# Kernel optimization log

Hardware: AMD Instinct MI355X
Metric: run time of the kernel (lower is better)

## Reference

```python
import jax, jax.numpy as jnp
from jax import lax
import numpy as np

ALPHA = 0.82
MAXITER = 10
N1_NODES = 2048
N2_NODES = 2048
K_ATTR = 64
EDGE_P = 0.004  # sparse-ish adjacency density


def setup_inputs() -> dict:
    key = jax.random.key(0)
    k1, k2, k3, k4 = jax.random.split(key, 4)
    A1 = (jax.random.uniform(k1, (N1_NODES, N1_NODES)) < EDGE_P).astype(jnp.float32)
    A1 = jnp.maximum(A1, A1.T)  # undirected 0/1 adjacency
    A2 = (jax.random.uniform(k2, (N2_NODES, N2_NODES)) < EDGE_P).astype(jnp.float32)
    A2 = jnp.maximum(A2, A2.T)
    N1 = jax.random.uniform(k3, (N1_NODES, K_ATTR), dtype=jnp.float32)
    N2 = jax.random.uniform(k4, (N2_NODES, K_ATTR), dtype=jnp.float32)
    # default prior (_get_H with path=None), normalized so sum ~= 1
    H = jnp.full((N2_NODES, N1_NODES), 1.0 / (N1_NODES * N2_NODES), dtype=jnp.float32)
    return {"A1": A1, "A2": A2, "N1": N1, "N2": N2, "H": H}


def _row_l2_normalize(N):
    nrm = jnp.sqrt(jnp.sum(N * N, axis=1, keepdims=True))
    return jnp.where(nrm > 0, N / jnp.where(nrm > 0, nrm, 1.0), 0.0)


def _final_forward(A1, A2, N1, N2, H, alpha=ALPHA, maxiter=MAXITER):
    # No edge attrs: L=1, E1=A1, E2=A2. T = 1/A^2 where A^2>0 (elementwise),
    # E <- E*T, so B = (E*A) = A*T*A.
    def masked_recip_sq(A):
        A2e = A * A
        return jnp.where(A2e > 0, 1.0 / jnp.where(A2e > 0, A2e, 1.0), 0.0)

    B1 = (A1 * masked_recip_sq(A1)) * A1  # (n1, n1)
    B2 = (A2 * masked_recip_sq(A2)) * A2  # (n2, n2)

    N1n = _row_l2_normalize(N1)  # (n1, K)
    N2n = _row_l2_normalize(N2)  # (n2, K)

    # Kronecker vectors laid out as (n1, n2) matrices (C-order == kron order):
    # N[i*n2+j] = sum_k N1[i,k]*N2[j,k]  -> N1n @ N2n.T
    Nm = N1n @ N2n.T  # (n1, n2)
    dm = (B1 @ N1n) @ (B2 @ N2n).T  # (n1, n2)
    D = Nm * dm
    DD = jnp.where(D > 0, lax.rsqrt(jnp.where(D > 0, D, 1.0)), 0.0)  # inf -> 0
    q = DD * Nm  # (n1, n2)

    # h = H.flatten('F') with H (n2,n1): as an (n1,n2) matrix this is H.T
    h = H.T  # (n1, n2)

    def step(s, _):
        # M = (q*s) reshaped (n2,n1) F-order == (q*s).T in our layout.
        # S = B2 @ M @ B1 (n2,n1); S.flatten('F') as (n1,n2) == B1.T @ (q*s) @ B2.T
        S_t = B1.T @ (q * s) @ B2.T  # (n1, n2)
        s_new = (1.0 - alpha) * h + alpha * q * S_t
        return s_new, None

    s, _ = lax.scan(step, h, None, length=maxiter)
    # original: s.reshape((n1, n2)) C-order -> exactly our layout
    return s  # (n1, n2) alignment matrix


def reference(A1, A2, N1, N2, H):
    return _final_forward(A1, A2, N1, N2, H)
```

## Files before the change

kernel.cpp:

```cpp
#include <hip/hip_runtime.h>

#define NMAT 2048
#define KATTR 64
#define CAP 128
#define NITER 10
#define NSTRIPE 128
#define LSTRIDE 9

typedef unsigned short ushort4v __attribute__((ext_vector_type(4)));

__device__ __forceinline__ unsigned short f2bf(float f) {
  unsigned u = __float_as_uint(f);
  return (unsigned short)((u + 0x7fff + ((u >> 16) & 1)) >> 16);
}
__device__ __forceinline__ float bf2f(unsigned short b) {
  return __uint_as_float((unsigned)b << 16);
}
__device__ __forceinline__ float bflo(unsigned v) {
  return __uint_as_float(v << 16);
}
__device__ __forceinline__ float bfhi(unsigned v) {
  return __uint_as_float(v & 0xffff0000u);
}
__device__ __forceinline__ int swz(int c) { return 4 * c + (((c >> 3) & 7) << 2); }
__device__ __forceinline__ size_t bidx(int i, int j) {
  return ((size_t)(j >> 4) * NMAT + i) * 16 + (j & 15);
}

__global__ __launch_bounds__(256) void k_build(
    const float* __restrict__ A, unsigned short* __restrict__ idx,
    unsigned short* __restrict__ idxT, int* __restrict__ cnt) {
  __shared__ int lcnt;
  int r = blockIdx.x;
  if (threadIdx.x == 0) lcnt = 0;
  __syncthreads();
  const float* row = A + (size_t)r * NMAT;
  for (int c = threadIdx.x; c < NMAT; c += 256) {
    if (row[c] != 0.0f) {
      int p = atomicAdd(&lcnt, 1);
      if (p < CAP) {
        idx[r * CAP + p] = (unsigned short)c;
        if (idxT) idxT[(size_t)p * NMAT + r] = (unsigned short)c;
      }
    }
  }
  __syncthreads();
  if (threadIdx.x == 0) cnt[r] = lcnt < CAP ? lcnt : CAP;
}

__global__ __launch_bounds__(256) void k_norm(const float* __restrict__ Nin,
                                              float* __restrict__ Nout) {
  int row = blockIdx.x * 4 + (threadIdx.x >> 6);
  int lane = threadIdx.x & 63;
  float v = Nin[(size_t)row * KATTR + lane];
  float ss = v * v;
#pragma unroll
  for (int o = 32; o > 0; o >>= 1) ss += __shfl_xor(ss, o);
  float nrm = sqrtf(ss);
  Nout[(size_t)row * KATTR + lane] = (nrm > 0.f) ? v / nrm : 0.f;
}

__global__ void k_gatherN(const unsigned short* __restrict__ idx,
                          const int* __restrict__ cnt,
                          const float* __restrict__ Nn,
                          float* __restrict__ C) {
  int i = blockIdx.x;
  int lane = threadIdx.x;
  int nn = cnt[i];
  const unsigned short* ip = idx + i * CAP;
  float acc = 0.f;
  for (int t = 0; t < nn; ++t) {
    int k = ip[t];
    acc += Nn[(size_t)k * KATTR + lane];
  }
  C[(size_t)i * KATTR + lane] = acc;
}

__global__ __launch_bounds__(256) void k_transpose(const float* __restrict__ H,
                                                   float* __restrict__ Ht) {
  __shared__ float tile[64][65];
  int j0 = blockIdx.x * 64;
  int i0 = blockIdx.y * 64;
  int c = threadIdx.x & 63;
  int r0 = threadIdx.x >> 6;
  for (int r = r0; r < 64; r += 4)
    tile[r][c] = H[(size_t)(j0 + r) * NMAT + i0 + c];
  __syncthreads();
  for (int r = r0; r < 64; r += 4)
    Ht[(size_t)(i0 + r) * NMAT + j0 + c] = tile[c][r];
}

__global__ __launch_bounds__(256) void k_q(
    const float* __restrict__ N1n, const float* __restrict__ C1,
    const float* __restrict__ N2n, const float* __restrict__ C2,
    const float* __restrict__ Ht, float* __restrict__ q,
    float* __restrict__ Q2, unsigned short* __restrict__ Mblk,
    unsigned short* __restrict__ M0base) {
  __shared__ float sA[64][68];
  __shared__ float sB[64][68];
  int i0 = blockIdx.y * 64, j0 = blockIdx.x * 64;
  int c = threadIdx.x & 63, r0 = threadIdx.x >> 6;
  int tx = threadIdx.x & 15, ty = threadIdx.x >> 4;
  const float alpha = 0.82f;

  float nmv[4][4] = {};
  float dmv[4][4] = {};

  for (int r = r0; r < 64; r += 4) {
    sA[c][r] = N1n[(size_t)(i0 + r) * KATTR + c];
    sB[c][r] = N2n[(size_t)(j0 + r) * KATTR + c];
  }
  __syncthreads();
#pragma unroll 4
  for (int k = 0; k < 64; ++k) {
    float4 a = *(const float4*)&sA[k][ty * 4];
    float4 b = *(const float4*)&sB[k][tx * 4];
    float av[4] = {a.x, a.y, a.z, a.w};
    float bv[4] = {b.x, b.y, b.z, b.w};
#pragma unroll
    for (int ii = 0; ii < 4; ++ii)
#pragma unroll
      for (int jj = 0; jj < 4; ++jj)
        nmv[ii][jj] = fmaf(av[ii], bv[jj], nmv[ii][jj]);
  }
  __syncthreads();
  for (int r = r0; r < 64; r += 4) {
    sA[c][r] = C1[(size_t)(i0 + r) * KATTR + c];
    sB[c][r] = C2[(size_t)(j0 + r) * KATTR + c];
  }
  __syncthreads();
#pragma unroll 4
  for (int k = 0; k < 64; ++k) {
    float4 a = *(const float4*)&sA[k][ty * 4];
    float4 b = *(const float4*)&sB[k][tx * 4];
    float av[4] = {a.x, a.y, a.z, a.w};
    float bv[4] = {b.x, b.y, b.z, b.w};
#pragma unroll
    for (int ii = 0; ii < 4; ++ii)
#pragma unroll
      for (int jj = 0; jj < 4; ++jj)
        dmv[ii][jj] = fmaf(av[ii], bv[jj], dmv[ii][jj]);
  }

#pragma unroll
  for (int ii = 0; ii < 4; ++ii) {
    int i = i0 + ty * 4 + ii;
    int jb = j0 + tx * 4;
    size_t base = (size_t)i * NMAT + jb;
    float4 hv = *(const float4*)&Ht[base];
    float hvv[4] = {hv.x, hv.y, hv.z, hv.w};
    float qv[4], q2v[4];
    ushort4v mv, m0v;
#pragma unroll
    for (int jj = 0; jj < 4; ++jj) {
      float nmx = nmv[ii][jj];
      float D = nmx * dmv[ii][jj];
      float qq = (D > 0.f) ? nmx * rsqrtf(D) : 0.f;
      qv[jj] = qq;
      q2v[jj] = alpha * qq * qq;
      float m0 = qq * hvv[jj];
      mv[jj] = f2bf(m0);
      m0v[jj] = f2bf((1.0f - alpha) * m0);
    }
    *(float4*)&q[base] = make_float4(qv[0], qv[1], qv[2], qv[3]);
    *(float4*)&Q2[base] = make_float4(q2v[0], q2v[1], q2v[2], q2v[3]);
    *(ushort4v*)&Mblk[bidx(i, jb)] = mv;
    *(ushort4v*)&M0base[base] = m0v;
  }
}

__global__ __launch_bounds__(1024, 8) void k1s(
    const unsigned short* __restrict__ idx1, const int* __restrict__ cnt1,
    const unsigned short* __restrict__ Mblk, float* __restrict__ T1) {
  __shared__ unsigned lds[NMAT * LSTRIDE];
  int stripe = blockIdx.x & (NSTRIPE - 1);
  int chunk = blockIdx.x >> 7;
  int tid = threadIdx.x;
  const unsigned* src = (const unsigned*)(Mblk + (size_t)stripe * NMAT * 16);
#pragma unroll
  for (int p = 0; p < 4; ++p) {
    int e = p * 4096 + tid * 4;
    uint4 v = *(const uint4*)(src + e);
    int row = e >> 3;
    int cc = e & 7;
    lds[row * LSTRIDE + cc] = v.x;
    lds[row * LSTRIDE + cc + 1] = v.y;
    lds[row * LSTRIDE + cc + 2] = v.z;
    lds[row * LSTRIDE + cc + 3] = v.w;
  }
  __syncthreads();

  int i = chunk * 512 + (tid >> 1);
  int h = tid & 1;
  int nn = cnt1[i];
  const unsigned short* ip = idx1 + i * CAP;
  float a0 = 0, a1 = 0, a2 = 0, a3 = 0, a4 = 0, a5 = 0, a6 = 0, a7 = 0;
  int t = 0;
  for (; t + 2 <= nn; t += 2) {
    unsigned pr = *(const unsigned*)(ip + t);
    int ka = (int)(pr & 0xffff) * LSTRIDE + h * 4;
    int kb = (int)(pr >> 16) * LSTRIDE + h * 4;
    unsigned w0 = lds[ka], w1 = lds[ka + 1], w2 = lds[ka + 2], w3 = lds[ka + 3];
    unsigned x0 = lds[kb], x1 = lds[kb + 1], x2 = lds[kb + 2], x3 = lds[kb + 3];
    a0 += bflo(w0) + bflo(x0); a1 += bfhi(w0) + bfhi(x0);
    a2 += bflo(w1) + bflo(x1); a3 += bfhi(w1) + bfhi(x1);
    a4 += bflo(w2) + bflo(x2); a5 += bfhi(w2) + bfhi(x2);
    a6 += bflo(w3) + bflo(x3); a7 += bfhi(w3) + bfhi(x3);
  }
  if (t < nn) {
    int ka = (int)ip[t] * LSTRIDE + h * 4;
    unsigned w0 = lds[ka], w1 = lds[ka + 1], w2 = lds[ka + 2], w3 = lds[ka + 3];
    a0 += bflo(w0); a1 += bfhi(w0);
    a2 += bflo(w1); a3 += bfhi(w1);
    a4 += bflo(w2); a5 += bfhi(w2);
    a6 += bflo(w3); a7 += bfhi(w3);
  }
  float* dst = T1 + (size_t)i * NMAT + stripe * 16 + h * 8;
  *(float4*)dst = make_float4(a0, a1, a2, a3);
  *(float4*)(dst + 4) = make_float4(a4, a5, a6, a7);
}

__global__ __launch_bounds__(1024, 8) void k2s(
    const unsigned short* __restrict__ idx2T, const int* __restrict__ cnt2,
    const float* __restrict__ T1, const float* __restrict__ Q2,
    const unsigned short* __restrict__ M0base,
    unsigned short* __restrict__ Moutb, float* __restrict__ MoutF,
    int out32) {
  __shared__ float lds[4 * NMAT + 32];
  int i0 = blockIdx.x * 4;
  int tid = threadIdx.x;
  int c0 = tid * 2;
  float2 v[4];
#pragma unroll
  for (int r = 0; r < 4; ++r)
    v[r] = *(const float2*)(T1 + (size_t)(i0 + r) * NMAT + c0);
  *(float4*)&lds[swz(c0)] = make_float4(v[0].x, v[1].x, v[2].x, v[3].x);
  *(float4*)&lds[swz(c0 + 1)] = make_float4(v[0].y, v[1].y, v[2].y, v[3].y);
  __syncthreads();

#pragma unroll
  for (int jj = 0; jj < 2; ++jj) {
    int j = jj * 1024 + tid;
    int nn = cnt2[j];
    const unsigned short* ip = idx2T + j;
    float s0 = 0.f, s1 = 0.f, s2 = 0.f, s3 = 0.f;
    float u0 = 0.f, u1 = 0.f, u2 = 0.f, u3 = 0.f;
    int t = 0;
    for (; t + 4 <= nn; t += 4) {
      int ka = ip[(size_t)t * NMAT];
      int kb = ip[(size_t)(t + 1) * NMAT];
      int kc = ip[(size_t)(t + 2) * NMAT];
      int kd = ip[(size_t)(t + 3) * NMAT];
      float4 va = *(const float4*)&lds[swz(ka)];
      float4 vb = *(const float4*)&lds[swz(kb)];
      float4 vc = *(const float4*)&lds[swz(kc)];
      float4 vd = *(const float4*)&lds[swz(kd)];
      s0 += va.x + vc.x; s1 += va.y + vc.y;
      s2 += va.z + vc.z; s3 += va.w + vc.w;
      u0 += vb.x + vd.x; u1 += vb.y + vd.y;
      u2 += vb.z + vd.z; u3 += vb.w + vd.w;
    }
    for (; t < nn; ++t) {
      int ka = ip[(size_t)t * NMAT];
      float4 va = *(const float4*)&lds[swz(ka)];
      s0 += va.x; s1 += va.y; s2 += va.z; s3 += va.w;
    }
    float sa[4] = {s0 + u0, s1 + u1, s2 + u2, s3 + u3};
    if (out32) {
#pragma unroll
      for (int r = 0; r < 4; ++r) {
        size_t off = (size_t)(i0 + r) * NMAT + j;
        MoutF[off] = fmaf(Q2[off], sa[r], bf2f(M0base[off]));
      }
    } else {
#pragma unroll
      for (int r = 0; r < 4; ++r) {
        size_t off = (size_t)(i0 + r) * NMAT + j;
        Moutb[bidx(i0 + r, j)] = f2bf(fmaf(Q2[off], sa[r], bf2f(M0base[off])));
      }
    }
  }
}

__global__ __launch_bounds__(1024, 8) void k_iter(
    const unsigned short* __restrict__ idx1, const int* __restrict__ cnt1,
    const unsigned short* __restrict__ idx2T, const int* __restrict__ cnt2,
    const float* __restrict__ MinF, const float* __restrict__ q,
    const float* __restrict__ Ht, float* __restrict__ sout) {
  __shared__ float lds[4 * NMAT + 32];
  int i0 = blockIdx.x * 4;
  int tid = threadIdx.x;
  int c0 = tid * 2;

  float acc[4][2];
#pragma unroll
  for (int r = 0; r < 4; ++r) {
    int nn = cnt1[i0 + r];
    const unsigned short* ip = idx1 + (i0 + r) * CAP;
    float a0 = 0.f, a1 = 0.f;
    float b0 = 0.f, b1 = 0.f;
    int t = 0;
    for (; t + 4 <= nn; t += 4) {
      uint2 pk = *(const uint2*)(ip + t);
      int k0 = pk.x & 0xffff, k1 = pk.x >> 16;
      int k2 = pk.y & 0xffff, k3 = pk.y >> 16;
      float2 v0 = *(const float2*)(MinF + (size_t)k0 * NMAT + c0);
      float2 v1 = *(const float2*)(MinF + (size_t)k1 * NMAT + c0);
      float2 v2 = *(const float2*)(MinF + (size_t)k2 * NMAT + c0);
      float2 v3 = *(const float2*)(MinF + (size_t)k3 * NMAT + c0);
      a0 += v0.x + v1.x; a1 += v0.y + v1.y;
      b0 += v2.x + v3.x; b1 += v2.y + v3.y;
    }
    for (; t < nn; ++t) {
      float2 v0 = *(const float2*)(MinF + (size_t)ip[t] * NMAT + c0);
      a0 += v0.x; a1 += v0.y;
    }
    acc[r][0] = a0 + b0;
    acc[r][1] = a1 + b1;
  }
  *(float4*)&lds[swz(c0)] =
      make_float4(acc[0][0], acc[1][0], acc[2][0], acc[3][0]);
  *(float4*)&lds[swz(c0 + 1)] =
      make_float4(acc[0][1], acc[1][1], acc[2][1], acc[3][1]);
  __syncthreads();

  const float alpha = 0.82f;
  const float oma = 1.0f - alpha;
#pragma unroll
  for (int jj = 0; jj < 2; ++jj) {
    int j = jj * 1024 + tid;
    int nn = cnt2[j];
    const unsigned short* ip = idx2T + j;
    float s0 = 0.f, s1 = 0.f, s2 = 0.f, s3 = 0.f;
    float u0 = 0.f, u1 = 0.f, u2 = 0.f, u3 = 0.f;
    int t = 0;
    for (; t + 4 <= nn; t += 4) {
      int ka = ip[(size_t)t * NMAT];
      int kb = ip[(size_t)(t + 1) * NMAT];
      int kc = ip[(size_t)(t + 2) * NMAT];
      int kd = ip[(size_t)(t + 3) * NMAT];
      float4 va = *(const float4*)&lds[swz(ka)];
      float4 vb = *(const float4*)&lds[swz(kb)];
      float4 vc = *(const float4*)&lds[swz(kc)];
      float4 vd = *(const float4*)&lds[swz(kd)];
      s0 += va.x + vc.x; s1 += va.y + vc.y;
      s2 += va.z + vc.z; s3 += va.w + vc.w;
      u0 += vb.x + vd.x; u1 += vb.y + vd.y;
      u2 += vb.z + vd.z; u3 += vb.w + vd.w;
    }
    for (; t < nn; ++t) {
      int ka = ip[(size_t)t * NMAT];
      float4 va = *(const float4*)&lds[swz(ka)];
      s0 += va.x; s1 += va.y; s2 += va.z; s3 += va.w;
    }
    float sa[4] = {s0 + u0, s1 + u1, s2 + u2, s3 + u3};
#pragma unroll
    for (int r = 0; r < 4; ++r) {
      size_t off = (size_t)(i0 + r) * NMAT + j;
      sout[off] = oma * Ht[off] + alpha * q[off] * sa[r];
    }
  }
}

extern "C" void kernel_launch(void* const* d_in, const int* in_sizes, int n_in,
                              void* d_out, int out_size, void* d_ws,
                              size_t ws_size, hipStream_t stream) {
  const float* A1 = (const float*)d_in[0];
  const float* A2 = (const float*)d_in[1];
  const float* N1 = (const float*)d_in[2];
  const float* N2 = (const float*)d_in[3];
  const float* H = (const float*)d_in[4];
  float* s_out = (float*)d_out;

  char* p = (char*)d_ws;
  auto take = [&](size_t bytes) {
    char* r = p;
    p += (bytes + 255) & ~(size_t)255;
    return r;
  };
  unsigned short* idx1 = (unsigned short*)take((size_t)NMAT * CAP * 2);
  unsigned short* idx2 = (unsigned short*)take((size_t)NMAT * CAP * 2);
  unsigned short* idx2T = (unsigned short*)take((size_t)CAP * NMAT * 2);
  int* cnt1 = (int*)take((size_t)NMAT * 4);
  int* cnt2 = (int*)take((size_t)NMAT * 4);
  float* N1n = (float*)take((size_t)NMAT * KATTR * 4);
  float* N2n = (float*)take((size_t)NMAT * KATTR * 4);
  float* C1 = (float*)take((size_t)NMAT * KATTR * 4);
  float* C2 = (float*)take((size_t)NMAT * KATTR * 4);
  float* Ht = (float*)take((size_t)NMAT * NMAT * 4);
  float* q = (float*)take((size_t)NMAT * NMAT * 4);
  float* Q2 = (float*)take((size_t)NMAT * NMAT * 4);
  unsigned short* Mb0 = (unsigned short*)take((size_t)NMAT * NMAT * 2);
  unsigned short* Mb1 = (unsigned short*)take((size_t)NMAT * NMAT * 2);
  unsigned short* M0b = (unsigned short*)take((size_t)NMAT * NMAT * 2);
  float* Mf = (float*)take((size_t)NMAT * NMAT * 4);
  float* T1 = (float*)take((size_t)NMAT * NMAT * 4);
  if ((size_t)(p - (char*)d_ws) > ws_size) return;

  k_build<<<NMAT, 256, 0, stream>>>(A1, idx1, (unsigned short*)nullptr, cnt1);
  k_build<<<NMAT, 256, 0, stream>>>(A2, idx2, idx2T, cnt2);
  k_norm<<<NMAT / 4, 256, 0, stream>>>(N1, N1n);
  k_norm<<<NMAT / 4, 256, 0, stream>>>(N2, N2n);
  k_gatherN<<<NMAT, 64, 0, stream>>>(idx1, cnt1, N1n, C1);
  k_gatherN<<<NMAT, 64, 0, stream>>>(idx2, cnt2, N2n, C2);
  k_transpose<<<dim3(32, 32), 256, 0, stream>>>(H, Ht);
  k_q<<<dim3(32, 32), 256, 0, stream>>>(N1n, C1, N2n, C2, Ht, q, Q2, Mb0,
                                        M0b);
  for (int it = 0; it < NITER - 1; ++it) {
    const unsigned short* Min = (it & 1) ? Mb1 : Mb0;
    unsigned short* Mout = (it & 1) ? Mb0 : Mb1;
    int out32 = (it == NITER - 2) ? 1 : 0;
    k1s<<<4 * NSTRIPE, 1024, 0, stream>>>(idx1, cnt1, Min, T1);
    k2s<<<NMAT / 4, 1024, 0, stream>>>(idx2T, cnt2, T1, Q2, M0b, Mout, Mf,
                                       out32);
  }
  k_iter<<<NMAT / 4, 1024, 0, stream>>>(idx1, cnt1, idx2T, cnt2, Mf, q, Ht,
                                        s_out);
}
```

Before: 474.2 us.

## Sort rows by degree for balanced warps and replace final gather kernel

```diff
diff --git a/kernel.cpp b/kernel.cpp
--- a/kernel.cpp
+++ b/kernel.cpp
@@ -5,6 +5,7 @@
 #define CAP 128
 #define NITER 10
 #define NSTRIPE 128
+#define NSTRIPEF 256
 #define LSTRIDE 9
 
 typedef unsigned short ushort4v __attribute__((ext_vector_type(4)));
@@ -25,6 +26,9 @@
 __device__ __forceinline__ int swz(int c) { return 4 * c + (((c >> 3) & 7) << 2); }
 __device__ __forceinline__ size_t bidx(int i, int j) {
   return ((size_t)(j >> 4) * NMAT + i) * 16 + (j & 15);
+}
+__device__ __forceinline__ size_t bidx32(int i, int j) {
+  return ((size_t)(j >> 3) * NMAT + i) * 8 + (j & 7);
 }
 
 __global__ __launch_bounds__(256) void k_build(
@@ -46,6 +50,31 @@
   }
   __syncthreads();
   if (threadIdx.x == 0) cnt[r] = lcnt < CAP ? lcnt : CAP;
+}
+
+__global__ __launch_bounds__(1024) void k_sort(const int* __restrict__ cnt,
+                                               unsigned short* __restrict__ perm) {
+  __shared__ int hist[CAP + 1];
+  __shared__ int base[CAP + 1];
+  int tid = threadIdx.x;
+  if (tid <= CAP) hist[tid] = 0;
+  __syncthreads();
+  for (int r = tid; r < NMAT; r += 1024) atomicAdd(&hist[cnt[r]], 1);
+  __syncthreads();
+  if (tid == 0) {
+    int acc = 0;
+    for (int b = 0; b <= CAP; ++b) {
+      base[b] = acc;
+      acc += hist[b];
+      hist[b] = 0;
+    }
+  }
+  __syncthreads();
+  for (int r = tid; r < NMAT; r += 1024) {
+    int b = cnt[r];
+    int pos = base[b] + atomicAdd(&hist[b], 1);
+    perm[pos] = (unsigned short)r;
+  }
 }
 
 __global__ __launch_bounds__(256) void k_norm(const float* __restrict__ Nin,
@@ -171,6 +200,7 @@
 
 __global__ __launch_bounds__(1024, 8) void k1s(
     const unsigned short* __restrict__ idx1, const int* __restrict__ cnt1,
+    const unsigned short* __restrict__ perm1,
     const unsigned short* __restrict__ Mblk, float* __restrict__ T1) {
   __shared__ unsigned lds[NMAT * LSTRIDE];
   int stripe = blockIdx.x & (NSTRIPE - 1);
@@ -190,7 +220,7 @@
   }
   __syncthreads();
 
-  int i = chunk * 512 + (tid >> 1);
+  int i = perm1[chunk * 512 + (tid >> 1)];
   int h = tid & 1;
   int nn = cnt1[i];
   const unsigned short* ip = idx1 + i * CAP;
@@ -220,13 +250,61 @@
   *(float4*)(dst + 4) = make_float4(a4, a5, a6, a7);
 }
 
+__global__ __launch_bounds__(1024, 8) void k1sf(
+    const unsigned short* __restrict__ idx1, const int* __restrict__ cnt1,
+    const unsigned short* __restrict__ perm1, const float* __restrict__ Mfb,
+    float* __restrict__ T1) {
+  __shared__ unsigned lds[NMAT * LSTRIDE];
+  int stripe = blockIdx.x & (NSTRIPEF - 1);
+  int chunk = blockIdx.x >> 8;
+  int tid = threadIdx.x;
+  const unsigned* src = (const unsigned*)(Mfb + (size_t)stripe * NMAT * 8);
+#pragma unroll
+  for (int p = 0; p < 4; ++p) {
+    int e = p * 4096 + tid * 4;
+    uint4 v = *(const uint4*)(src + e);
+    int row = e >> 3;
+    int cc = e & 7;
+    lds[row * LSTRIDE + cc] = v.x;
+    lds[row * LSTRIDE + cc + 1] = v.y;
+    lds[row * LSTRIDE + cc + 2] = v.z;
+    lds[row * LSTRIDE + cc + 3] = v.w;
+  }
+  __syncthreads();
+
+  int i = perm1[chunk * 512 + (tid >> 1)];
+  int h = tid & 1;
+  int nn = cnt1[i];
+  const unsigned short* ip = idx1 + i * CAP;
+  float a0 = 0, a1 = 0, a2 = 0, a3 = 0;
+  float b0 = 0, b1 = 0, b2 = 0, b3 = 0;
+  int t = 0;
+  for (; t + 2 <= nn; t += 2) {
+    unsigned pr = *(const unsigned*)(ip + t);
+    int ka = (int)(pr & 0xffff) * LSTRIDE + h * 4;
+    int kb = (int)(pr >> 16) * LSTRIDE + h * 4;
+    a0 += __uint_as_float(lds[ka]);     a1 += __uint_as_float(lds[ka + 1]);
+    a2 += __uint_as_float(lds[ka + 2]); a3 += __uint_as_float(lds[ka + 3]);
+    b0 += __uint_as_float(lds[kb]);     b1 += __uint_as_float(lds[kb + 1]);
+    b2 += __uint_as_float(lds[kb + 2]); b3 += __uint_as_float(lds[kb + 3]);
+  }
+  if (t < nn) {
+    int ka = (int)ip[t] * LSTRIDE + h * 4;
+    a0 += __uint_as_float(lds[ka]);     a1 += __uint_as_float(lds[ka + 1]);
+    a2 += __uint_as_float(lds[ka + 2]); a3 += __uint_as_float(lds[ka + 3]);
+  }
+  float* dst = T1 + (size_t)i * NMAT + stripe * 8 + h * 4;
+  *(float4*)dst = make_float4(a0 + b0, a1 + b1, a2 + b2, a3 + b3);
+}
+
 __global__ __launch_bounds__(1024, 8) void k2s(
     const unsigned short* __restrict__ idx2T, const int* __restrict__ cnt2,
-    const float* __restrict__ T1, const float* __restrict__ Q2,
-    const unsigned short* __restrict__ M0base,
+    const unsigned short* __restrict__ perm2, const float* __restrict__ T1,
+    const float* __restrict__ Q2, const unsigned short* __restrict__ M0base,
     unsigned short* __restrict__ Moutb, float* __restrict__ MoutF,
     int out32) {
   __shared__ float lds[4 * NMAT + 32];
+  __shared__ float sS[4 * NMAT];
   int i0 = blockIdx.x * 4;
   int tid = threadIdx.x;
   int c0 = tid * 2;
@@ -240,7 +318,7 @@
 
 #pragma unroll
   for (int jj = 0; jj < 2; ++jj) {
-    int j = jj * 1024 + tid;
+    int j = perm2[jj * 1024 + tid];
     int nn = cnt2[j];
     const unsigned short* ip = idx2T + j;
     float s0 = 0.f, s1 = 0.f, s2 = 0.f, s3 = 0.f;
@@ -265,12 +343,22 @@
       float4 va = *(const float4*)&lds[swz(ka)];
       s0 += va.x; s1 += va.y; s2 += va.z; s3 += va.w;
     }
-    float sa[4] = {s0 + u0, s1 + u1, s2 + u2, s3 + u3};
+    sS[j] = s0 + u0;
+    sS[NMAT + j] = s1 + u1;
+    sS[2 * NMAT + j] = s2 + u2;
+    sS[3 * NMAT + j] = s3 + u3;
+  }
+  __syncthreads();
+
+#pragma unroll
+  for (int jj = 0; jj < 2; ++jj) {
+    int j = jj * 1024 + tid;
+    float sa[4] = {sS[j], sS[NMAT + j], sS[2 * NMAT + j], sS[3 * NMAT + j]};
     if (out32) {
 #pragma unroll
       for (int r = 0; r < 4; ++r) {
         size_t off = (size_t)(i0 + r) * NMAT + j;
-        MoutF[off] = fmaf(Q2[off], sa[r], bf2f(M0base[off]));
+        MoutF[bidx32(i0 + r, j)] = fmaf(Q2[off], sa[r], bf2f(M0base[off]));
       }
     } else {
 #pragma unroll
@@ -282,53 +370,27 @@
   }
 }
 
-__global__ __launch_bounds__(1024, 8) void k_iter(
-    const unsigned short* __restrict__ idx1, const int* __restrict__ cnt1,
+__global__ __launch_bounds__(1024, 8) void k2fin(
     const unsigned short* __restrict__ idx2T, const int* __restrict__ cnt2,
-    const float* __restrict__ MinF, const float* __restrict__ q,
-    const float* __restrict__ Ht, float* __restrict__ sout) {
+    const unsigned short* __restrict__ perm2, const float* __restrict__ T1,
+    const float* __restrict__ q, const float* __restrict__ Ht,
+    float* __restrict__ sout) {
   __shared__ float lds[4 * NMAT + 32];
+  __shared__ float sS[4 * NMAT];
   int i0 = blockIdx.x * 4;
   int tid = threadIdx.x;
   int c0 = tid * 2;
-
-  float acc[4][2];
-#pragma unroll
-  for (int r = 0; r < 4; ++r) {
-    int nn = cnt1[i0 + r];
-    const unsigned short* ip = idx1 + (i0 + r) * CAP;
-    float a0 = 0.f, a1 = 0.f;
-    float b0 = 0.f, b1 = 0.f;
-    int t = 0;
-    for (; t + 4 <= nn; t += 4) {
-      uint2 pk = *(const uint2*)(ip + t);
-      int k0 = pk.x & 0xffff, k1 = pk.x >> 16;
-      int k2 = pk.y & 0xffff, k3 = pk.y >> 16;
-      float2 v0 = *(const float2*)(MinF + (size_t)k0 * NMAT + c0);
-      float2 v1 = *(const float2*)(MinF + (size_t)k1 * NMAT + c0);
-      float2 v2 = *(const float2*)(MinF + (size_t)k2 * NMAT + c0);
-      float2 v3 = *(const float2*)(MinF + (size_t)k3 * NMAT + c0);
-      a0 += v0.x + v1.x; a1 += v0.y + v1.y;
-      b0 += v2.x + v3.x; b1 += v2.y + v3.y;
-    }
-    for (; t < nn; ++t) {
-      float2 v0 = *(const float2*)(MinF + (size_t)ip[t] * NMAT + c0);
-      a0 += v0.x; a1 += v0.y;
-    }
-    acc[r][0] = a0 + b0;
-    acc[r][1] = a1 + b1;
-  }
-  *(float4*)&lds[swz(c0)] =
-      make_float4(acc[0][0], acc[1][0], acc[2][0], acc[3][0]);
-  *(float4*)&lds[swz(c0 + 1)] =
-      make_float4(acc[0][1], acc[1][1], acc[2][1], acc[3][1]);
-  __syncthreads();
-
-  const float alpha = 0.82f;
-  const float oma = 1.0f - alpha;
+  float2 v[4];
+#pragma unroll
+  for (int r = 0; r < 4; ++r)
+    v[r] = *(const float2*)(T1 + (size_t)(i0 + r) * NMAT + c0);
+  *(float4*)&lds[swz(c0)] = make_float4(v[0].x, v[1].x, v[2].x, v[3].x);
+  *(float4*)&lds[swz(c0 + 1)] = make_float4(v[0].y, v[1].y, v[2].y, v[3].y);
+  __syncthreads();
+
 #pragma unroll
   for (int jj = 0; jj < 2; ++jj) {
-    int j = jj * 1024 + tid;
+    int j = perm2[jj * 1024 + tid];
     int nn = cnt2[j];
     const unsigned short* ip = idx2T + j;
     float s0 = 0.f, s1 = 0.f, s2 = 0.f, s3 = 0.f;
@@ -353,7 +415,19 @@
       float4 va = *(const float4*)&lds[swz(ka)];
       s0 += va.x; s1 += va.y; s2 += va.z; s3 += va.w;
     }
-    float sa[4] = {s0 + u0, s1 + u1, s2 + u2, s3 + u3};
+    sS[j] = s0 + u0;
+    sS[NMAT + j] = s1 + u1;
+    sS[2 * NMAT + j] = s2 + u2;
+    sS[3 * NMAT + j] = s3 + u3;
+  }
+  __syncthreads();
+
+  const float alpha = 0.82f;
+  const float oma = 1.0f - alpha;
+#pragma unroll
+  for (int jj = 0; jj < 2; ++jj) {
+    int j = jj * 1024 + tid;
+    float sa[4] = {sS[j], sS[NMAT + j], sS[2 * NMAT + j], sS[3 * NMAT + j]};
 #pragma unroll
     for (int r = 0; r < 4; ++r) {
       size_t off = (size_t)(i0 + r) * NMAT + j;
@@ -383,6 +457,8 @@
   unsigned short* idx2T = (unsigned short*)take((size_t)CAP * NMAT * 2);
   int* cnt1 = (int*)take((size_t)NMAT * 4);
   int* cnt2 = (int*)take((size_t)NMAT * 4);
+  unsigned short* perm1 = (unsigned short*)take((size_t)NMAT * 2);
+  unsigned short* perm2 = (unsigned short*)take((size_t)NMAT * 2);
   float* N1n = (float*)take((size_t)NMAT * KATTR * 4);
   float* N2n = (float*)take((size_t)NMAT * KATTR * 4);
   float* C1 = (float*)take((size_t)NMAT * KATTR * 4);
@@ -399,6 +475,8 @@
 
   k_build<<<NMAT, 256, 0, stream>>>(A1, idx1, (unsigned short*)nullptr, cnt1);
   k_build<<<NMAT, 256, 0, stream>>>(A2, idx2, idx2T, cnt2);
+  k_sort<<<1, 1024, 0, stream>>>(cnt1, perm1);
+  k_sort<<<1, 1024, 0, stream>>>(cnt2, perm2);
   k_norm<<<NMAT / 4, 256, 0, stream>>>(N1, N1n);
   k_norm<<<NMAT / 4, 256, 0, stream>>>(N2, N2n);
   k_gatherN<<<NMAT, 64, 0, stream>>>(idx1, cnt1, N1n, C1);
@@ -410,10 +488,10 @@
     const unsigned short* Min = (it & 1) ? Mb1 : Mb0;
     unsigned short* Mout = (it & 1) ? Mb0 : Mb1;
     int out32 = (it == NITER - 2) ? 1 : 0;
-    k1s<<<4 * NSTRIPE, 1024, 0, stream>>>(idx1, cnt1, Min, T1);
-    k2s<<<NMAT / 4, 1024, 0, stream>>>(idx2T, cnt2, T1, Q2, M0b, Mout, Mf,
-                                       out32);
-  }
-  k_iter<<<NMAT / 4, 1024, 0, stream>>>(idx1, cnt1, idx2T, cnt2, Mf, q, Ht,
-                                        s_out);
-}
+    k1s<<<4 * NSTRIPE, 1024, 0, stream>>>(idx1, cnt1, perm1, Min, T1);
+    k2s<<<NMAT / 4, 1024, 0, stream>>>(idx2T, cnt2, perm2, T1, Q2, M0b, Mout,
+                                       Mf, out32);
+  }
+  k1sf<<<4 * NSTRIPEF, 1024, 0, stream>>>(idx1, cnt1, perm1, Mf, T1);
+  k2fin<<<NMAT / 4, 1024, 0, stream>>>(idx2T, cnt2, perm2, T1, q, Ht, s_out);
+}
```

Result: slower. 566.6 us (+19.5%).
